# Performance work log

Measured on AMD Instinct MI355X. Metric: run time of the kernel, lower is better.

## Reference

```python
import jax, jax.numpy as jnp
from jax import lax
import numpy as np

S, D, L, H, C = 128, 3, 16, 512, 10
B, T = 32, 16384


def setup_inputs() -> dict:
    key = jax.random.key(0)
    ks = jax.random.split(key, 6)
    x = jax.random.normal(ks[0], (B, D, T), dtype=jnp.float32)
    shapelets = jax.random.normal(ks[1], (S, 1, D, L), dtype=jnp.float32)  # OIHW, one per shapelet
    W1 = jax.random.normal(ks[2], (H, S), dtype=jnp.float32) * (1.0 / np.sqrt(S))
    b1 = jnp.zeros((H,), dtype=jnp.float32)
    W2 = jax.random.normal(ks[3], (C, H), dtype=jnp.float32) * (1.0 / np.sqrt(H))
    b2 = jnp.zeros((C,), dtype=jnp.float32)
    return {"x": x, "shapelets": shapelets, "W1": W1, "b1": b1, "W2": W2, "b2": b2}


def reference(x, shapelets, W1, b1, W2, b2):
    # x: [B, D, T] -> [B, 1, D, T]; kernels slide only over time (full-height conv).
    x4 = x[:, None, :, :]
    dn = ("NCHW", "OIHW", "NCHW")
    ones_k = jnp.ones((1, 1, shapelets.shape[2], shapelets.shape[3]), dtype=x.dtype)
    # ||window||^2 per sliding window: [B, 1, 1, Tout]
    window_square = lax.conv_general_dilated(x4 * x4, ones_k, (1, 1), "VALID", dimension_numbers=dn)
    # all cross-correlations in one grouped conv: [B, S, 1, Tout]
    cross_corr = lax.conv_general_dilated(x4, shapelets, (1, 1), "VALID", dimension_numbers=dn)
    shapelet_square = jnp.sum(shapelets * shapelets, axis=(1, 2, 3))  # [S]
    # squared distance per (shapelet, window), min-reduced over windows
    dist = window_square + shapelet_square[None, :, None, None] - 2.0 * cross_corr  # [B, S, 1, Tout]
    distance = jnp.min(dist, axis=(2, 3))  # [B, S]
    h = jax.nn.relu(distance @ W1.T + b1)
    classification = h @ W2.T + b2
    return (distance, classification)
```

## Files before the change

kernel.cpp:

```cpp
#include <hip/hip_runtime.h>
#include <hip/hip_bf16.h>

#define Bn 32
#define Tn 16384
#define Ln 16
#define Sn 128
#define Hn 512
#define Cn 10
#define Kn 48
#define TOUT 16369
#define CH 1024
#define NCH 16
#define XLEN 1048

typedef short  s16x8  __attribute__((ext_vector_type(8)));
typedef float  f32x16 __attribute__((ext_vector_type(16)));

__device__ __forceinline__ unsigned short f2bf(float f) {
    union { float f; unsigned int u; } v; v.f = f;
    unsigned int r = v.u + 0x7FFF + ((v.u >> 16) & 1);
    return (unsigned short)(r >> 16);
}

__global__ __launch_bounds__(256, 2) void dist_kernel(const float* __restrict__ x,
                                                      const float* __restrict__ sh,
                                                      float* __restrict__ partial) {
    __shared__ unsigned short xph[24 * XLEN];
    __shared__ float winsq_lds[CH];
    __shared__ float wavemin[4 * Sn];

    const int tid   = threadIdx.x;
    const int b     = blockIdx.x >> 4;
    const int chunk = blockIdx.x & 15;
    const int tb    = chunk * CH;
    const int lane  = tid & 63;
    const int w     = tid >> 6;
    const int n     = lane & 31;
    const int h     = lane >> 5;

    float* shf = (float*)xph;
    {
        const float4* s4 = (const float4*)sh;
        for (int i = tid; i < Sn * Kn / 4; i += 256) ((float4*)shf)[i] = s4[i];
    }
    __syncthreads();

    s16x8 bfr[3][4];
    float shsqv[4];
    #pragma unroll
    for (int st = 0; st < 4; ++st) {
        const int s = st * 32 + n;
        const float* row = shf + s * Kn;
        float q = 0.f;
        #pragma unroll
        for (int k = 0; k < Kn; ++k) q = fmaf(row[k], row[k], q);
        shsqv[st] = q;
        #pragma unroll
        for (int kk = 0; kk < 3; ++kk)
            #pragma unroll
            for (int j = 0; j < 8; ++j)
                bfr[kk][st][j] = (short)f2bf(-2.0f * row[kk * 16 + 8 * h + j]);
    }
    __syncthreads();

    const float* xb = x + b * 3 * Tn;
    for (int p = 0; p < 8; ++p) {
        for (int idx = tid; idx < 3 * (XLEN / 2); idx += 256) {
            const int d = idx / (XLEN / 2);
            const int e = idx - d * (XLEN / 2);
            const int u = 2 * e;
            const int t0 = tb + u + p;
            const float f0 = (t0     < Tn) ? xb[d * Tn + t0]     : 0.f;
            const float f1 = (t0 + 1 < Tn) ? xb[d * Tn + t0 + 1] : 0.f;
            const unsigned int packed = (unsigned int)f2bf(f0) | ((unsigned int)f2bf(f1) << 16);
            *(unsigned int*)(void*)&xph[(p * 3 + d) * XLEN + u] = packed;
        }
    }

    {
        const int i0 = tid * 4;
        const int t0 = tb + i0;
        float q0 = 0.f, q1 = 0.f, q2 = 0.f, q3 = 0.f;
        #pragma unroll
        for (int d = 0; d < 3; ++d) {
            const float* xd = xb + d * Tn + t0;
            float wv[19];
            #pragma unroll
            for (int l = 0; l < 19; ++l) wv[l] = (t0 + l < Tn) ? xd[l] : 0.f;
            float s = 0.f;
            #pragma unroll
            for (int l = 0; l < 16; ++l) s = fmaf(wv[l], wv[l], s);
            q0 += s;
            s = s - wv[0] * wv[0] + wv[16] * wv[16]; q1 += s;
            s = s - wv[1] * wv[1] + wv[17] * wv[17]; q2 += s;
            s = s - wv[2] * wv[2] + wv[18] * wv[18]; q3 += s;
        }
        winsq_lds[i0    ] = (tb + i0     >= TOUT) ? 1e30f : q0;
        winsq_lds[i0 + 1] = (tb + i0 + 1 >= TOUT) ? 1e30f : q1;
        winsq_lds[i0 + 2] = (tb + i0 + 2 >= TOUT) ? 1e30f : q2;
        winsq_lds[i0 + 3] = (tb + i0 + 3 >= TOUT) ? 1e30f : q3;
    }
    __syncthreads();

    f32x16 zero16 = {0.f, 0.f, 0.f, 0.f, 0.f, 0.f, 0.f, 0.f,
                     0.f, 0.f, 0.f, 0.f, 0.f, 0.f, 0.f, 0.f};
    float mcol[4] = {1e30f, 1e30f, 1e30f, 1e30f};
    const int g = w >> 1;
    const int rbase = 8 * (w & 1);

    for (int rr = 0; rr < 8; ++rr) {
        const int i  = (g << 9) + rbase + rr;
        const int p  = i & 7;
        const int ib = i - p;
        const int u0 = ib + 16 * n + 8 * h;
        const unsigned short* xp = &xph[p * 3 * XLEN + u0];
        const s16x8 a0 = *(const s16x8*)(const void*)(xp);
        const s16x8 a1 = *(const s16x8*)(const void*)(xp + XLEN);
        const s16x8 a2 = *(const s16x8*)(const void*)(xp + 2 * XLEN);

        f32x16 acc[4];
        #pragma unroll
        for (int st = 0; st < 4; ++st) {
            acc[st] = __builtin_amdgcn_mfma_f32_32x32x16_bf16(a0, bfr[0][st], zero16, 0, 0, 0);
            acc[st] = __builtin_amdgcn_mfma_f32_32x32x16_bf16(a1, bfr[1][st], acc[st], 0, 0, 0);
            acc[st] = __builtin_amdgcn_mfma_f32_32x32x16_bf16(a2, bfr[2][st], acc[st], 0, 0, 0);
        }

        float wq[16];
        #pragma unroll
        for (int reg = 0; reg < 16; ++reg) {
            const int row = (reg & 3) + 8 * (reg >> 2) + 4 * h;
            wq[reg] = winsq_lds[i + 16 * row];
        }
        #pragma unroll
        for (int st = 0; st < 4; ++st)
            #pragma unroll
            for (int reg = 0; reg < 16; ++reg) {
                const float v = acc[st][reg] + wq[reg] + shsqv[st];
                mcol[st] = fminf(mcol[st], v);
            }
    }

    #pragma unroll
    for (int st = 0; st < 4; ++st) {
        float mm = mcol[st];
        mm = fminf(mm, __shfl_xor(mm, 32, 64));
        if (h == 0) wavemin[w * Sn + st * 32 + n] = mm;
    }
    __syncthreads();
    if (tid < Sn) {
        const float mm = fminf(fminf(wavemin[tid], wavemin[Sn + tid]),
                               fminf(wavemin[2 * Sn + tid], wavemin[3 * Sn + tid]));
        partial[(b * NCH + chunk) * Sn + tid] = mm;
    }
}

__global__ __launch_bounds__(512) void mlp_kernel(const float* __restrict__ partial,
                                                  const float* __restrict__ W1,
                                                  const float* __restrict__ b1,
                                                  const float* __restrict__ W2,
                                                  const float* __restrict__ b2,
                                                  float* __restrict__ out) {
    __shared__ float db[Sn];
    __shared__ float hb[Hn];
    __shared__ float part[Cn][32];
    const int b = blockIdx.x, tid = threadIdx.x;

    if (tid < Sn) {
        float mm = 1e30f;
        #pragma unroll
        for (int ch = 0; ch < NCH; ++ch)
            mm = fminf(mm, partial[(b * NCH + ch) * Sn + tid]);
        db[tid] = mm;
        out[b * Sn + tid] = mm;
    }
    __syncthreads();

    float a = b1[tid];
    const float4* w1r = (const float4*)(W1 + tid * Sn);
    const float4* dbv = (const float4*)db;
    #pragma unroll 8
    for (int i = 0; i < Sn / 4; ++i) {
        const float4 wv = w1r[i];
        const float4 dv = dbv[i];
        a = fmaf(dv.x, wv.x, a); a = fmaf(dv.y, wv.y, a);
        a = fmaf(dv.z, wv.z, a); a = fmaf(dv.w, wv.w, a);
    }
    hb[tid] = fmaxf(a, 0.0f);
    __syncthreads();

    if (tid < Cn * 32) {
        const int c = tid >> 5, p = tid & 31;
        float acc = 0.f;
        #pragma unroll
        for (int i = 0; i < Hn / 32; ++i)
            acc = fmaf(hb[p + 32 * i], W2[c * Hn + p + 32 * i], acc);
        part[c][p] = acc;
    }
    __syncthreads();
    if (tid < Cn) {
        float acc = b2[tid];
        for (int p = 0; p < 32; ++p) acc += part[tid][p];
        out[Bn * Sn + b * Cn + tid] = acc;
    }
}

extern "C" void kernel_launch(void* const* d_in, const int* in_sizes, int n_in,
                              void* d_out, int out_size, void* d_ws, size_t ws_size,
                              hipStream_t stream) {
    const float* x  = (const float*)d_in[0];
    const float* sh = (const float*)d_in[1];
    const float* W1 = (const float*)d_in[2];
    const float* b1 = (const float*)d_in[3];
    const float* W2 = (const float*)d_in[4];
    const float* b2 = (const float*)d_in[5];
    float* out = (float*)d_out;
    float* partial = (float*)d_ws;

    dist_kernel<<<Bn * NCH, 256, 0, stream>>>(x, sh, partial);
    mlp_kernel<<<Bn, 512, 0, stream>>>(partial, W1, b1, W2, b2, out);
}
```

Measured before the change: 104.4 us.

## Halve time chunk, build shifted bf16 phases in LDS, hoist shapelet norm

Halves the time chunk per block (doubling the grid) and raises the occupancy hint to 3 blocks per CU. The eight shifted bf16 copies of x are now derived from one global load via in-LDS word shifts rather than eight separate global reads. The shapelet-norm add moves out of the inner min loop, and the shapelet LDS stage uses a padded pitch to avoid bank conflicts. The MLP kernel's chunk reduction is split across all 512 threads to handle the larger partial count; the cost is more blocks, redundant halo work, and an extra LDS pass and sync.

```diff
diff --git a/kernel.cpp b/kernel.cpp
--- a/kernel.cpp
+++ b/kernel.cpp
@@ -9,9 +9,10 @@
 #define Cn 10
 #define Kn 48
 #define TOUT 16369
-#define CH 1024
-#define NCH 16
-#define XLEN 1048
+#define CH 512
+#define NCH 32
+#define XLEN 560
+#define SPITCH 52
 
 typedef short  s16x8  __attribute__((ext_vector_type(8)));
 typedef float  f32x16 __attribute__((ext_vector_type(16)));
@@ -22,7 +23,7 @@
     return (unsigned short)(r >> 16);
 }
 
-__global__ __launch_bounds__(256, 2) void dist_kernel(const float* __restrict__ x,
+__global__ __launch_bounds__(256, 3) void dist_kernel(const float* __restrict__ x,
                                                       const float* __restrict__ sh,
                                                       float* __restrict__ partial) {
     __shared__ unsigned short xph[24 * XLEN];
@@ -30,8 +31,8 @@
     __shared__ float wavemin[4 * Sn];
 
     const int tid   = threadIdx.x;
-    const int b     = blockIdx.x >> 4;
-    const int chunk = blockIdx.x & 15;
+    const int b     = blockIdx.x >> 5;
+    const int chunk = blockIdx.x & 31;
     const int tb    = chunk * CH;
     const int lane  = tid & 63;
     const int w     = tid >> 6;
@@ -41,7 +42,10 @@
     float* shf = (float*)xph;
     {
         const float4* s4 = (const float4*)sh;
-        for (int i = tid; i < Sn * Kn / 4; i += 256) ((float4*)shf)[i] = s4[i];
+        for (int i = tid; i < Sn * (Kn / 4); i += 256) {
+            const int s = i / 12, q = i - s * 12;
+            ((float4*)(shf + s * SPITCH))[q] = s4[i];
+        }
     }
     __syncthreads();
 
@@ -50,7 +54,7 @@
     #pragma unroll
     for (int st = 0; st < 4; ++st) {
         const int s = st * 32 + n;
-        const float* row = shf + s * Kn;
+        const float* row = shf + s * SPITCH;
         float q = 0.f;
         #pragma unroll
         for (int k = 0; k < Kn; ++k) q = fmaf(row[k], row[k], q);
@@ -64,86 +68,98 @@
     __syncthreads();
 
     const float* xb = x + b * 3 * Tn;
-    for (int p = 0; p < 8; ++p) {
-        for (int idx = tid; idx < 3 * (XLEN / 2); idx += 256) {
-            const int d = idx / (XLEN / 2);
-            const int e = idx - d * (XLEN / 2);
-            const int u = 2 * e;
-            const int t0 = tb + u + p;
-            const float f0 = (t0     < Tn) ? xb[d * Tn + t0]     : 0.f;
-            const float f1 = (t0 + 1 < Tn) ? xb[d * Tn + t0 + 1] : 0.f;
-            const unsigned int packed = (unsigned int)f2bf(f0) | ((unsigned int)f2bf(f1) << 16);
-            *(unsigned int*)(void*)&xph[(p * 3 + d) * XLEN + u] = packed;
-        }
+    unsigned int* xpu = (unsigned int*)xph;
+    for (int idx = tid; idx < 3 * 272; idx += 256) {
+        const int d = idx / 272, e = idx - d * 272;
+        const int t0 = tb + 2 * e;
+        const float f0 = (t0     < Tn) ? xb[d * Tn + t0]     : 0.f;
+        const float f1 = (t0 + 1 < Tn) ? xb[d * Tn + t0 + 1] : 0.f;
+        xpu[d * (XLEN / 2) + e] = (unsigned int)f2bf(f0) | ((unsigned int)f2bf(f1) << 16);
     }
 
     {
-        const int i0 = tid * 4;
+        const int i0 = tid * 2;
         const int t0 = tb + i0;
-        float q0 = 0.f, q1 = 0.f, q2 = 0.f, q3 = 0.f;
+        float q0 = 0.f, q1 = 0.f;
         #pragma unroll
         for (int d = 0; d < 3; ++d) {
             const float* xd = xb + d * Tn + t0;
-            float wv[19];
-            #pragma unroll
-            for (int l = 0; l < 19; ++l) wv[l] = (t0 + l < Tn) ? xd[l] : 0.f;
+            float wv[17];
+            #pragma unroll
+            for (int l = 0; l < 17; ++l) wv[l] = (t0 + l < Tn) ? xd[l] : 0.f;
             float s = 0.f;
             #pragma unroll
             for (int l = 0; l < 16; ++l) s = fmaf(wv[l], wv[l], s);
             q0 += s;
-            s = s - wv[0] * wv[0] + wv[16] * wv[16]; q1 += s;
-            s = s - wv[1] * wv[1] + wv[17] * wv[17]; q2 += s;
-            s = s - wv[2] * wv[2] + wv[18] * wv[18]; q3 += s;
-        }
-        winsq_lds[i0    ] = (tb + i0     >= TOUT) ? 1e30f : q0;
-        winsq_lds[i0 + 1] = (tb + i0 + 1 >= TOUT) ? 1e30f : q1;
-        winsq_lds[i0 + 2] = (tb + i0 + 2 >= TOUT) ? 1e30f : q2;
-        winsq_lds[i0 + 3] = (tb + i0 + 3 >= TOUT) ? 1e30f : q3;
-    }
-    __syncthreads();
-
-    f32x16 zero16 = {0.f, 0.f, 0.f, 0.f, 0.f, 0.f, 0.f, 0.f,
-                     0.f, 0.f, 0.f, 0.f, 0.f, 0.f, 0.f, 0.f};
+            s = s - wv[0] * wv[0] + wv[16] * wv[16];
+            q1 += s;
+        }
+        winsq_lds[i0    ] = (t0     >= TOUT) ? 1e30f : q0;
+        winsq_lds[i0 + 1] = (t0 + 1 >= TOUT) ? 1e30f : q1;
+    }
+    __syncthreads();
+
+    for (int p = 1; p < 8; ++p) {
+        const int half = p >> 1;
+        for (int idx = tid; idx < 3 * 268; idx += 256) {
+            const int d = idx / 268, e = idx - d * 268;
+            const unsigned int* src = xpu + d * (XLEN / 2);
+            unsigned int val;
+            if (p & 1) {
+                const unsigned int A = src[e + half];
+                const unsigned int B = src[e + half + 1];
+                val = (A >> 16) | (B << 16);
+            } else {
+                val = src[e + half];
+            }
+            xpu[(p * 3 + d) * (XLEN / 2) + e] = val;
+        }
+    }
+    __syncthreads();
+
+    const f32x16 zero16 = {0.f, 0.f, 0.f, 0.f, 0.f, 0.f, 0.f, 0.f,
+                           0.f, 0.f, 0.f, 0.f, 0.f, 0.f, 0.f, 0.f};
     float mcol[4] = {1e30f, 1e30f, 1e30f, 1e30f};
-    const int g = w >> 1;
-    const int rbase = 8 * (w & 1);
-
-    for (int rr = 0; rr < 8; ++rr) {
-        const int i  = (g << 9) + rbase + rr;
+
+    for (int rr = 0; rr < 4; ++rr) {
+        const int i  = 4 * w + rr;
         const int p  = i & 7;
-        const int ib = i - p;
+        const int ib = i & ~7;
         const int u0 = ib + 16 * n + 8 * h;
         const unsigned short* xp = &xph[p * 3 * XLEN + u0];
         const s16x8 a0 = *(const s16x8*)(const void*)(xp);
         const s16x8 a1 = *(const s16x8*)(const void*)(xp + XLEN);
         const s16x8 a2 = *(const s16x8*)(const void*)(xp + 2 * XLEN);
 
-        f32x16 acc[4];
-        #pragma unroll
-        for (int st = 0; st < 4; ++st) {
-            acc[st] = __builtin_amdgcn_mfma_f32_32x32x16_bf16(a0, bfr[0][st], zero16, 0, 0, 0);
-            acc[st] = __builtin_amdgcn_mfma_f32_32x32x16_bf16(a1, bfr[1][st], acc[st], 0, 0, 0);
-            acc[st] = __builtin_amdgcn_mfma_f32_32x32x16_bf16(a2, bfr[2][st], acc[st], 0, 0, 0);
-        }
-
-        float wq[16];
-        #pragma unroll
-        for (int reg = 0; reg < 16; ++reg) {
-            const int row = (reg & 3) + 8 * (reg >> 2) + 4 * h;
-            wq[reg] = winsq_lds[i + 16 * row];
-        }
-        #pragma unroll
-        for (int st = 0; st < 4; ++st)
-            #pragma unroll
-            for (int reg = 0; reg < 16; ++reg) {
-                const float v = acc[st][reg] + wq[reg] + shsqv[st];
-                mcol[st] = fminf(mcol[st], v);
+        #pragma unroll
+        for (int sp = 0; sp < 2; ++sp) {
+            f32x16 acc[2];
+            #pragma unroll
+            for (int q = 0; q < 2; ++q) {
+                const int st = sp * 2 + q;
+                acc[q] = __builtin_amdgcn_mfma_f32_32x32x16_bf16(a0, bfr[0][st], zero16, 0, 0, 0);
+                acc[q] = __builtin_amdgcn_mfma_f32_32x32x16_bf16(a1, bfr[1][st], acc[q], 0, 0, 0);
+                acc[q] = __builtin_amdgcn_mfma_f32_32x32x16_bf16(a2, bfr[2][st], acc[q], 0, 0, 0);
             }
+            #pragma unroll
+            for (int reg = 0; reg < 16; reg += 2) {
+                const int row0 = (reg & 3) + 8 * (reg >> 2) + 4 * h;
+                const float w0 = winsq_lds[i + 16 * row0];
+                const float w1 = winsq_lds[i + 16 * (row0 + 1)];
+                #pragma unroll
+                for (int q = 0; q < 2; ++q) {
+                    const int st = sp * 2 + q;
+                    const float u = acc[q][reg]     + w0;
+                    const float v = acc[q][reg + 1] + w1;
+                    mcol[st] = fminf(fminf(mcol[st], u), v);
+                }
+            }
+        }
     }
 
     #pragma unroll
     for (int st = 0; st < 4; ++st) {
-        float mm = mcol[st];
+        float mm = mcol[st] + shsqv[st];
         mm = fminf(mm, __shfl_xor(mm, 32, 64));
         if (h == 0) wavemin[w * Sn + st * 32 + n] = mm;
     }
@@ -161,25 +177,33 @@
                                                   const float* __restrict__ W2,
                                                   const float* __restrict__ b2,
                                                   float* __restrict__ out) {
+    __shared__ float pmin[4][Sn];
     __shared__ float db[Sn];
     __shared__ float hb[Hn];
     __shared__ float part[Cn][32];
     const int b = blockIdx.x, tid = threadIdx.x;
 
+    {
+        const int s = tid & 127, g = tid >> 7;
+        const float* pp = partial + (b * NCH + g * 8) * Sn + s;
+        float m = pp[0];
+        #pragma unroll
+        for (int c = 1; c < 8; ++c) m = fminf(m, pp[c * Sn]);
+        pmin[g][s] = m;
+    }
+    __syncthreads();
     if (tid < Sn) {
-        float mm = 1e30f;
-        #pragma unroll
-        for (int ch = 0; ch < NCH; ++ch)
-            mm = fminf(mm, partial[(b * NCH + ch) * Sn + tid]);
-        db[tid] = mm;
-        out[b * Sn + tid] = mm;
+        const float m = fminf(fminf(pmin[0][tid], pmin[1][tid]),
+                              fminf(pmin[2][tid], pmin[3][tid]));
+        db[tid] = m;
+        out[b * Sn + tid] = m;
     }
     __syncthreads();
 
     float a = b1[tid];
     const float4* w1r = (const float4*)(W1 + tid * Sn);
     const float4* dbv = (const float4*)db;
-    #pragma unroll 8
+    #pragma unroll
     for (int i = 0; i < Sn / 4; ++i) {
         const float4 wv = w1r[i];
         const float4 dv = dbv[i];
@@ -200,6 +224,7 @@
     __syncthreads();
     if (tid < Cn) {
         float acc = b2[tid];
+        #pragma unroll
         for (int p = 0; p < 32; ++p) acc += part[tid][p];
         out[Bn * Sn + b * Cn + tid] = acc;
     }
```

After: 165.9 us. 1.59x slower.

## Swizzle LDS phase buffers, vectorize staging loads, and restructure window-square layout

Applied to the files above, without the earlier changes.

Replaces the scalar strided LDS staging of the eight phase-shifted bf16 copies of x with per-thread vectorized global loads, register-level shifting, and 16-byte stores into an XOR-swizzled LDS layout meant to avoid bank conflicts on the MFMA operand reads. Shapelet fragments are now loaded straight from global memory as float4, which drops the LDS round-trip and a barrier. The window-square table is transposed so each lane reads four float4s instead of sixteen scalars. The shapelet norm is moved out of the inner min loop and added once at the end. The MLP kernel's 16-way partial-min reduction is split across four thread groups. Together these add indexing complexity and boundary-special-case code paths in exchange for cheaper memory access.

```diff
diff --git a/kernel.cpp b/kernel.cpp
--- a/kernel.cpp
+++ b/kernel.cpp
@@ -11,7 +11,9 @@
 #define TOUT 16369
 #define CH 1024
 #define NCH 16
-#define XLEN 1048
+#define XLEN 1056
+#define XDW  (XLEN / 2)
+#define XGRP (XLEN / 8)
 
 typedef short  s16x8  __attribute__((ext_vector_type(8)));
 typedef float  f32x16 __attribute__((ext_vector_type(16)));
@@ -22,11 +24,13 @@
     return (unsigned short)(r >> 16);
 }
 
+__device__ __forceinline__ int swz(int g) { return g ^ ((g >> 3) & 7); }
+
 __global__ __launch_bounds__(256, 2) void dist_kernel(const float* __restrict__ x,
                                                       const float* __restrict__ sh,
                                                       float* __restrict__ partial) {
-    __shared__ unsigned short xph[24 * XLEN];
-    __shared__ float winsq_lds[CH];
+    __shared__ unsigned int xph[24 * XDW];
+    __shared__ float wsq[16 * 64];
     __shared__ float wavemin[4 * Sn];
 
     const int tid   = threadIdx.x;
@@ -37,56 +41,96 @@
     const int w     = tid >> 6;
     const int n     = lane & 31;
     const int h     = lane >> 5;
-
-    float* shf = (float*)xph;
-    {
-        const float4* s4 = (const float4*)sh;
-        for (int i = tid; i < Sn * Kn / 4; i += 256) ((float4*)shf)[i] = s4[i];
-    }
-    __syncthreads();
+    const bool interior = (tb + XLEN + 8) <= Tn;
 
     s16x8 bfr[3][4];
     float shsqv[4];
     #pragma unroll
     for (int st = 0; st < 4; ++st) {
-        const int s = st * 32 + n;
-        const float* row = shf + s * Kn;
+        const float4* row4 = (const float4*)(sh + (st * 32 + n) * Kn);
         float q = 0.f;
         #pragma unroll
-        for (int k = 0; k < Kn; ++k) q = fmaf(row[k], row[k], q);
+        for (int c = 0; c < 12; ++c) {
+            const float4 v = row4[c];
+            q = fmaf(v.x, v.x, q); q = fmaf(v.y, v.y, q);
+            q = fmaf(v.z, v.z, q); q = fmaf(v.w, v.w, q);
+        }
         shsqv[st] = q;
         #pragma unroll
-        for (int kk = 0; kk < 3; ++kk)
-            #pragma unroll
-            for (int j = 0; j < 8; ++j)
-                bfr[kk][st][j] = (short)f2bf(-2.0f * row[kk * 16 + 8 * h + j]);
-    }
-    __syncthreads();
-
-    const float* xb = x + b * 3 * Tn;
-    for (int p = 0; p < 8; ++p) {
-        for (int idx = tid; idx < 3 * (XLEN / 2); idx += 256) {
-            const int d = idx / (XLEN / 2);
-            const int e = idx - d * (XLEN / 2);
-            const int u = 2 * e;
-            const int t0 = tb + u + p;
-            const float f0 = (t0     < Tn) ? xb[d * Tn + t0]     : 0.f;
-            const float f1 = (t0 + 1 < Tn) ? xb[d * Tn + t0 + 1] : 0.f;
-            const unsigned int packed = (unsigned int)f2bf(f0) | ((unsigned int)f2bf(f1) << 16);
-            *(unsigned int*)(void*)&xph[(p * 3 + d) * XLEN + u] = packed;
+        for (int kk = 0; kk < 3; ++kk) {
+            const float4 va = row4[kk * 4 + 2 * h];
+            const float4 vb = row4[kk * 4 + 2 * h + 1];
+            bfr[kk][st][0] = (short)f2bf(-2.0f * va.x);
+            bfr[kk][st][1] = (short)f2bf(-2.0f * va.y);
+            bfr[kk][st][2] = (short)f2bf(-2.0f * va.z);
+            bfr[kk][st][3] = (short)f2bf(-2.0f * va.w);
+            bfr[kk][st][4] = (short)f2bf(-2.0f * vb.x);
+            bfr[kk][st][5] = (short)f2bf(-2.0f * vb.y);
+            bfr[kk][st][6] = (short)f2bf(-2.0f * vb.z);
+            bfr[kk][st][7] = (short)f2bf(-2.0f * vb.w);
+        }
+    }
+
+    if (tid < 198) {
+        const int ch = tid / 66, j = tid - ch * 66;
+        const float* xs = x + (b * 3 + ch) * Tn + tb + 16 * j;
+        float in[24];
+        if (interior) {
+            const float4* x4 = (const float4*)xs;
+            #pragma unroll
+            for (int q = 0; q < 6; ++q) {
+                const float4 v = x4[q];
+                in[4 * q] = v.x; in[4 * q + 1] = v.y; in[4 * q + 2] = v.z; in[4 * q + 3] = v.w;
+            }
+        } else {
+            #pragma unroll
+            for (int k = 0; k < 24; ++k) {
+                const int t = tb + 16 * j + k;
+                in[k] = (t < Tn) ? xs[k] : 0.f;
+            }
+        }
+        unsigned int r[12];
+        #pragma unroll
+        for (int q = 0; q < 12; ++q)
+            r[q] = (unsigned int)f2bf(in[2 * q]) | ((unsigned int)f2bf(in[2 * q + 1]) << 16);
+
+        #pragma unroll
+        for (int p = 0; p < 8; ++p) {
+            unsigned int v[8];
+            #pragma unroll
+            for (int e = 0; e < 8; ++e) {
+                const int o = 2 * e + p;
+                v[e] = (o & 1) ? ((r[o >> 1] >> 16) | (r[(o >> 1) + 1] << 16))
+                               : r[o >> 1];
+            }
+            const int gb = (p * 3 + ch) * XGRP + 2 * j;
+            uint4 lo = {v[0], v[1], v[2], v[3]};
+            uint4 hi4 = {v[4], v[5], v[6], v[7]};
+            *(uint4*)((char*)xph + (swz(gb)     << 4)) = lo;
+            *(uint4*)((char*)xph + (swz(gb + 1) << 4)) = hi4;
         }
     }
 
     {
-        const int i0 = tid * 4;
-        const int t0 = tb + i0;
+        const int t0 = 4 * tid;
         float q0 = 0.f, q1 = 0.f, q2 = 0.f, q3 = 0.f;
         #pragma unroll
-        for (int d = 0; d < 3; ++d) {
-            const float* xd = xb + d * Tn + t0;
+        for (int ch = 0; ch < 3; ++ch) {
+            const float* xd = x + (b * 3 + ch) * Tn + tb + t0;
             float wv[19];
-            #pragma unroll
-            for (int l = 0; l < 19; ++l) wv[l] = (t0 + l < Tn) ? xd[l] : 0.f;
+            if (interior) {
+                const float4* x4 = (const float4*)xd;
+                #pragma unroll
+                for (int q = 0; q < 4; ++q) {
+                    const float4 v = x4[q];
+                    wv[4 * q] = v.x; wv[4 * q + 1] = v.y; wv[4 * q + 2] = v.z; wv[4 * q + 3] = v.w;
+                }
+                wv[16] = xd[16]; wv[17] = xd[17]; wv[18] = xd[18];
+            } else {
+                #pragma unroll
+                for (int l = 0; l < 19; ++l)
+                    wv[l] = (tb + t0 + l < Tn) ? xd[l] : 0.f;
+            }
             float s = 0.f;
             #pragma unroll
             for (int l = 0; l < 16; ++l) s = fmaf(wv[l], wv[l], s);
@@ -95,28 +139,27 @@
             s = s - wv[1] * wv[1] + wv[17] * wv[17]; q2 += s;
             s = s - wv[2] * wv[2] + wv[18] * wv[18]; q3 += s;
         }
-        winsq_lds[i0    ] = (tb + i0     >= TOUT) ? 1e30f : q0;
-        winsq_lds[i0 + 1] = (tb + i0 + 1 >= TOUT) ? 1e30f : q1;
-        winsq_lds[i0 + 2] = (tb + i0 + 2 >= TOUT) ? 1e30f : q2;
-        winsq_lds[i0 + 3] = (tb + i0 + 3 >= TOUT) ? 1e30f : q3;
-    }
-    __syncthreads();
-
-    f32x16 zero16 = {0.f, 0.f, 0.f, 0.f, 0.f, 0.f, 0.f, 0.f,
-                     0.f, 0.f, 0.f, 0.f, 0.f, 0.f, 0.f, 0.f};
+        const float qs[4] = {q0, q1, q2, q3};
+        #pragma unroll
+        for (int c = 0; c < 4; ++c) {
+            const int t = t0 + c;
+            wsq[(t & 15) * 64 + (t >> 4)] = (tb + t >= TOUT) ? 1e30f : qs[c];
+        }
+    }
+    __syncthreads();
+
     float mcol[4] = {1e30f, 1e30f, 1e30f, 1e30f};
-    const int g = w >> 1;
-    const int rbase = 8 * (w & 1);
+    const f32x16 zero16 = {0.f, 0.f, 0.f, 0.f, 0.f, 0.f, 0.f, 0.f,
+                           0.f, 0.f, 0.f, 0.f, 0.f, 0.f, 0.f, 0.f};
 
     for (int rr = 0; rr < 8; ++rr) {
-        const int i  = (g << 9) + rbase + rr;
-        const int p  = i & 7;
-        const int ib = i - p;
-        const int u0 = ib + 16 * n + 8 * h;
-        const unsigned short* xp = &xph[p * 3 * XLEN + u0];
-        const s16x8 a0 = *(const s16x8*)(const void*)(xp);
-        const s16x8 a1 = *(const s16x8*)(const void*)(xp + XLEN);
-        const s16x8 a2 = *(const s16x8*)(const void*)(xp + 2 * XLEN);
+        const int tau = 8 * w + rr;
+        const int i   = (tau & 15) + ((tau >> 4) << 9);
+        const int p   = i & 7;
+        const int gb  = p * 3 * XGRP + (i >> 3) + 2 * n + h;
+        const s16x8 a0 = *(const s16x8*)((const char*)xph + (swz(gb)            << 4));
+        const s16x8 a1 = *(const s16x8*)((const char*)xph + (swz(gb + XGRP)     << 4));
+        const s16x8 a2 = *(const s16x8*)((const char*)xph + (swz(gb + 2 * XGRP) << 4));
 
         f32x16 acc[4];
         #pragma unroll
@@ -126,24 +169,25 @@
             acc[st] = __builtin_amdgcn_mfma_f32_32x32x16_bf16(a2, bfr[2][st], acc[st], 0, 0, 0);
         }
 
-        float wq[16];
-        #pragma unroll
-        for (int reg = 0; reg < 16; ++reg) {
-            const int row = (reg & 3) + 8 * (reg >> 2) + 4 * h;
-            wq[reg] = winsq_lds[i + 16 * row];
-        }
+        const int ilow = i & 15, ihi = i >> 9;
+        float4 wq[4];
+        #pragma unroll
+        for (int q = 0; q < 4; ++q)
+            wq[q] = *(const float4*)&wsq[ilow * 64 + 8 * q + 4 * h + 32 * ihi];
+
         #pragma unroll
         for (int st = 0; st < 4; ++st)
             #pragma unroll
-            for (int reg = 0; reg < 16; ++reg) {
-                const float v = acc[st][reg] + wq[reg] + shsqv[st];
-                mcol[st] = fminf(mcol[st], v);
+            for (int reg = 0; reg < 16; reg += 2) {
+                const float u = acc[st][reg]     + ((const float*)&wq[reg >> 2])[0 + (reg & 3)];
+                const float v = acc[st][reg + 1] + ((const float*)&wq[reg >> 2])[1 + (reg & 3)];
+                mcol[st] = fminf(fminf(mcol[st], u), v);
             }
     }
 
     #pragma unroll
     for (int st = 0; st < 4; ++st) {
-        float mm = mcol[st];
+        float mm = mcol[st] + shsqv[st];
         mm = fminf(mm, __shfl_xor(mm, 32, 64));
         if (h == 0) wavemin[w * Sn + st * 32 + n] = mm;
     }
@@ -161,25 +205,33 @@
                                                   const float* __restrict__ W2,
                                                   const float* __restrict__ b2,
                                                   float* __restrict__ out) {
+    __shared__ float pmin[4][Sn];
     __shared__ float db[Sn];
     __shared__ float hb[Hn];
     __shared__ float part[Cn][32];
     const int b = blockIdx.x, tid = threadIdx.x;
 
+    {
+        const int s = tid & 127, g = tid >> 7;
+        const float* pp = partial + (b * NCH + g * 4) * Sn + s;
+        float m = pp[0];
+        #pragma unroll
+        for (int c = 1; c < 4; ++c) m = fminf(m, pp[c * Sn]);
+        pmin[g][s] = m;
+    }
+    __syncthreads();
     if (tid < Sn) {
-        float mm = 1e30f;
-        #pragma unroll
-        for (int ch = 0; ch < NCH; ++ch)
-            mm = fminf(mm, partial[(b * NCH + ch) * Sn + tid]);
-        db[tid] = mm;
-        out[b * Sn + tid] = mm;
+        const float m = fminf(fminf(pmin[0][tid], pmin[1][tid]),
+                              fminf(pmin[2][tid], pmin[3][tid]));
+        db[tid] = m;
+        out[b * Sn + tid] = m;
     }
     __syncthreads();
 
     float a = b1[tid];
     const float4* w1r = (const float4*)(W1 + tid * Sn);
     const float4* dbv = (const float4*)db;
-    #pragma unroll 8
+    #pragma unroll
     for (int i = 0; i < Sn / 4; ++i) {
         const float4 wv = w1r[i];
         const float4 dv = dbv[i];
@@ -200,6 +252,7 @@
     __syncthreads();
     if (tid < Cn) {
         float acc = b2[tid];
+        #pragma unroll
         for (int p = 0; p < 32; ++p) acc += part[tid][p];
         out[Bn * Sn + b * Cn + tid] = acc;
     }
```

Measured after the change: 114.7 us. 1.1x slower.
